# Optimization experiments

Hardware: AMD Instinct MI355X
Metric: run time of the kernel (lower is better)

The kernel has to match this reference:

```python
import jax, jax.numpy as jnp
import numpy as np

D_MODEL = 1024
N_HEADS = 16
HEAD_DIM = D_MODEL // N_HEADS


def setup_inputs() -> dict:
    key = jax.random.key(0)
    ks = jax.random.split(key, 5)
    B, S = 4, 2048
    scale = 1.0 / np.sqrt(D_MODEL)
    return {
        "x": jax.random.normal(ks[0], (B, S, D_MODEL), dtype=jnp.float32),
        "wq": jax.random.normal(ks[1], (D_MODEL, D_MODEL), dtype=jnp.float32) * scale,
        "wk": jax.random.normal(ks[2], (D_MODEL, D_MODEL), dtype=jnp.float32) * scale,
        "wv": jax.random.normal(ks[3], (D_MODEL, D_MODEL), dtype=jnp.float32) * scale,
        "wo": jax.random.normal(ks[4], (D_MODEL, D_MODEL), dtype=jnp.float32) * scale,
    }


def reference(x, wq, wk, wv, wo):
    B, S, _ = x.shape
    # projections: x @ W.T, then split heads -> [B, H, S, hd]
    def split_heads(t):
        return t.reshape(B, S, N_HEADS, HEAD_DIM).transpose(0, 2, 1, 3)

    q = split_heads(x @ wq.T)
    k = split_heads(x @ wk.T)
    v = split_heads(x @ wv.T)

    # scores [B, H, S, S], causal mask, stable softmax
    score = jnp.einsum("bhqd,bhkd->bhqk", q, k) / np.sqrt(HEAD_DIM)
    causal = jnp.tril(jnp.ones((S, S), dtype=bool))
    score = jnp.where(causal, score, -jnp.inf)
    attn = jax.nn.softmax(score, axis=-1)

    out = jnp.einsum("bhqk,bhkd->bhqd", attn, v)
    out = out.transpose(0, 2, 1, 3).reshape(B, S, D_MODEL)
    return out @ wo.T
```

## Files before the change

kernel.cpp:

```cpp
#include <hip/hip_runtime.h>
#include <type_traits>


typedef unsigned short u16;
typedef __attribute__((ext_vector_type(8))) short s8;
typedef __attribute__((ext_vector_type(4))) float f4;

__device__ __forceinline__ u16 f2bf(float f) {
    union { float f; unsigned u; } v; v.f = f;
    unsigned r = v.u + 0x7fffu + ((v.u >> 16) & 1u);
    return (u16)(r >> 16);
}

__device__ __forceinline__ unsigned pack_bf2(float a, float b) {
    return __builtin_amdgcn_perm(__float_as_uint(b), __float_as_uint(a),
                                 0x07060302u);
}

__device__ __forceinline__ void cp16(const void* g, void* l) {
    __builtin_amdgcn_global_load_lds(
        (const __attribute__((address_space(1))) unsigned int*)g,
        (__attribute__((address_space(3))) unsigned int*)l, 16, 0, 0);
}

__device__ __forceinline__ s8 load8f(const float* p) {
    const float4 lo = *(const float4*)p;
    const float4 hi = *(const float4*)(p + 4);
    s8 r;
    r[0] = (short)f2bf(lo.x); r[1] = (short)f2bf(lo.y);
    r[2] = (short)f2bf(lo.z); r[3] = (short)f2bf(lo.w);
    r[4] = (short)f2bf(hi.x); r[5] = (short)f2bf(hi.y);
    r[6] = (short)f2bf(hi.z); r[7] = (short)f2bf(hi.w);
    return r;
}

__global__ __launch_bounds__(256)
void f32_to_bf16(const float* __restrict__ in, u16* __restrict__ out, int n8)
{
    const int i = blockIdx.x * 256 + threadIdx.x;
    if (i < n8) *(s8*)(out + (size_t)i * 8) = load8f(in + (size_t)i * 8);
}

__global__ __launch_bounds__(256)
void cvt_w3(const float* __restrict__ a, const float* __restrict__ b2,
            const float* __restrict__ c3, u16* __restrict__ o, int per)
{
    const int y = blockIdx.y;
    const float* src = (y == 0) ? a : ((y == 1) ? b2 : c3);
    u16* dst = o + (size_t)y * per;
    const int i = blockIdx.x * 256 + threadIdx.x;
    *(s8*)(dst + (size_t)i * 8) = load8f(src + (size_t)i * 8);
}

template<typename TC>
__global__ __launch_bounds__(256)
void gemm_bb(const u16* __restrict__ A,
             const u16* __restrict__ W0, const u16* __restrict__ W1,
             const u16* __restrict__ W2,
             TC* __restrict__ C0, TC* __restrict__ C1,
             u16* __restrict__ VT, int K, float cscale)
{
    __shared__ u16 As[128 * 32];
    __shared__ u16 Bs[128 * 32];

    const int t  = threadIdx.x;
    const int bm = blockIdx.x;
    const int nglob = blockIdx.y * 128;

    const u16* W; int nloc, mode;
    if (nglob < 1024)      { W = W0; nloc = nglob;        mode = 0; }
    else if (nglob < 2048) { W = W1; nloc = nglob - 1024; mode = 1; }
    else                   { W = W2; nloc = nglob - 2048; mode = 2; }

    const int lane = t & 63, w = t >> 6;
    const int wm = (w >> 1) * 64, wn = (w & 1) * 64;
    const int quad = lane >> 4, l16 = lane & 15;

    const int sc = (((lane & 3) ^ ((lane >> 3) & 3))) * 8;
    const int sr = w * 32 + (lane >> 2);
    const u16* Ag0 = A + (size_t)(bm * 128 + sr) * K + sc;
    const u16* Ag1 = Ag0 + (size_t)16 * K;
    const u16* Wg0 = W + (size_t)(nloc + sr) * K + sc;
    const u16* Wg1 = Wg0 + (size_t)16 * K;
    u16* Al0 = As + (w * 32) * 32;
    u16* Al1 = As + (w * 32 + 16) * 32;
    u16* Bl0 = Bs + (w * 32) * 32;
    u16* Bl1 = Bs + (w * 32 + 16) * 32;

    const int ca = (quad ^ ((l16 >> 1) & 3)) * 8;

    f4 acc[4][4];
    for (int i = 0; i < 4; i++)
        for (int j = 0; j < 4; j++)
            acc[i][j] = (f4){0.f, 0.f, 0.f, 0.f};

    for (int k0 = 0; k0 < K; k0 += 32) {
        __syncthreads();
        cp16(Ag0 + k0, Al0);
        cp16(Ag1 + k0, Al1);
        cp16(Wg0 + k0, Bl0);
        cp16(Wg1 + k0, Bl1);
        __syncthreads();

        s8 af[4], bf[4];
        for (int i = 0; i < 4; i++)
            af[i] = *(const s8*)&As[(wm + i * 16 + l16) * 32 + ca];
        for (int j = 0; j < 4; j++)
            bf[j] = *(const s8*)&Bs[(wn + j * 16 + l16) * 32 + ca];
        for (int i = 0; i < 4; i++)
            for (int j = 0; j < 4; j++)
                acc[i][j] = __builtin_amdgcn_mfma_f32_16x16x32_bf16(
                                af[i], bf[j], acc[i][j], 0, 0, 0);
    }

    if (mode == 2) {
        for (int i = 0; i < 4; i++) {
            const int row0 = bm * 128 + wm + i * 16 + quad * 4;
            const int b = row0 >> 11, s = row0 & 2047;
            for (int j = 0; j < 4; j++) {
                const int n = nloc + wn + j * 16 + l16;
                const int h = n >> 6, d = n & 63;
                unsigned lo = ((unsigned)f2bf(acc[i][j][1]) << 16) | f2bf(acc[i][j][0]);
                unsigned hi = ((unsigned)f2bf(acc[i][j][3]) << 16) | f2bf(acc[i][j][2]);
                *(uint2*)(VT + ((size_t)((b * 16 + h) * 64 + d)) * 2048 + s) =
                    make_uint2(lo, hi);
            }
        }
    } else {
        TC* C = (mode == 0) ? C0 : C1;
        const float cs = (mode == 0) ? cscale : 1.0f;
        for (int i = 0; i < 4; i++) {
            const int row = bm * 128 + wm + i * 16 + quad * 4;
            for (int j = 0; j < 4; j++) {
                const int col = nloc + wn + j * 16 + l16;
                for (int r = 0; r < 4; r++) {
                    const float val = acc[i][j][r] * cs;
                    if constexpr (std::is_same<TC, float>::value)
                        C[(size_t)(row + r) * 1024 + col] = val;
                    else
                        C[(size_t)(row + r) * 1024 + col] = f2bf(val);
                }
            }
        }
    }
}

#define PSTR 72

__global__ __launch_bounds__(256)
void attn256(const u16* __restrict__ Q, const u16* __restrict__ K,
             const u16* __restrict__ Vt, u16* __restrict__ O)
{
    __shared__ u16 Ks[64 * 64];
    __shared__ u16 Vs[64 * 64];
    __shared__ u16 Ps[4][64 * PSTR];

    const int h  = blockIdx.x;
    const int b  = blockIdx.y;
    const int QBMAP[8] = {7, 6, 5, 4, 0, 1, 2, 3};
    const int qb = QBMAP[blockIdx.z];

    const int t = threadIdx.x, lane = t & 63, w = t >> 6;
    const int quad = lane >> 4, l16 = lane & 15;
    const int colH = h * 64;
    const size_t rowQ0 = (size_t)b * 2048 + qb * 256 + w * 64;

    s8 qf[4][2];
    for (int i = 0; i < 4; i++)
        for (int kk = 0; kk < 2; kk++)
            qf[i][kk] = *(const s8*)&Q[(rowQ0 + i * 16 + l16) * 1024 +
                                       colH + kk * 32 + quad * 8];

    s8 ones;
    for (int e = 0; e < 8; e++) ones[e] = (short)0x3F80;

    f4 o_acc[4][4];
    f4 l_acc[4];
    for (int i = 0; i < 4; i++) {
        l_acc[i] = (f4){0.f, 0.f, 0.f, 0.f};
        for (int j = 0; j < 4; j++)
            o_acc[i][j] = (f4){0.f, 0.f, 0.f, 0.f};
    }

    const int ktmax_blk = qb * 4 + 4;
    const int ktmax_w   = qb * 4 + w + 1;

    const int vrow = lane >> 3;
    const int scc  = ((lane & 7) ^ vrow) * 8;
    const int r0   = w * 16 + vrow;
    const u16* Kg0 = K  + ((size_t)b * 2048 + r0) * 1024 + colH + scc;
    const u16* Kg1 = Kg0 + (size_t)8 * 1024;
    const u16* Vg0 = Vt + ((size_t)(b * 16 + h) * 64 + r0) * 2048 + scc;
    const u16* Vg1 = Vg0 + (size_t)8 * 2048;
    const int lds_off = (lane & 7) * 8;
    u16* Kl0 = Ks + (w * 16 + vrow) * 64 + lds_off;
    u16* Kl1 = Ks + (w * 16 + 8 + vrow) * 64 + lds_off;
    u16* Vl0 = Vs + (w * 16 + vrow) * 64 + lds_off;
    u16* Vl1 = Vs + (w * 16 + 8 + vrow) * 64 + lds_off;

    s8 kr0 = *(const s8*)(Kg0);
    s8 kr1 = *(const s8*)(Kg1);
    s8 vr0 = *(const s8*)(Vg0);
    s8 vr1 = *(const s8*)(Vg1);

    for (int kt = 0; kt < ktmax_blk; ++kt) {
        __syncthreads();
        *(s8*)Kl0 = kr0;
        *(s8*)Kl1 = kr1;
        *(s8*)Vl0 = vr0;
        *(s8*)Vl1 = vr1;
        __syncthreads();

        if (kt + 1 < ktmax_blk) {
            kr0 = *(const s8*)(Kg0 + (size_t)(kt + 1) * 65536);
            kr1 = *(const s8*)(Kg1 + (size_t)(kt + 1) * 65536);
            vr0 = *(const s8*)(Vg0 + (kt + 1) * 64);
            vr1 = *(const s8*)(Vg1 + (kt + 1) * 64);
        }

        if (kt < ktmax_w) {
            f4 sa[4][4];
            for (int j = 0; j < 4; j++)
                for (int i = 0; i < 4; i++)
                    sa[j][i] = (f4){0.f, 0.f, 0.f, 0.f};
            for (int kk = 0; kk < 2; kk++) {
                s8 kf[4];
                for (int j = 0; j < 4; j++)
                    kf[j] = *(const s8*)&Ks[(j * 16 + l16) * 64 +
                                            (((kk * 4 + quad) ^ (l16 & 7)) * 8)];
                for (int j = 0; j < 4; j++)
                    for (int i = 0; i < 4; i++)
                        sa[j][i] = __builtin_amdgcn_mfma_f32_16x16x32_bf16(
                                       kf[j], qf[i][kk], sa[j][i], 0, 0, 0);
            }

            const bool diag = (kt == ktmax_w - 1);
            for (int i = 0; i < 4; i++) {
                const int q_l = i * 16 + l16;
                for (int j = 0; j < 4; j++) {
                    const int kv0 = j * 16 + quad * 4;
                    float p0 = exp2f(sa[j][i][0]);
                    float p1 = exp2f(sa[j][i][1]);
                    float p2 = exp2f(sa[j][i][2]);
                    float p3 = exp2f(sa[j][i][3]);
                    if (diag) {
                        if (kv0 + 0 > q_l) p0 = 0.f;
                        if (kv0 + 1 > q_l) p1 = 0.f;
                        if (kv0 + 2 > q_l) p2 = 0.f;
                        if (kv0 + 3 > q_l) p3 = 0.f;
                    }
                    *(uint2*)&Ps[w][q_l * PSTR + kv0] =
                        make_uint2(pack_bf2(p0, p1), pack_bf2(p2, p3));
                }
            }

            for (int kk = 0; kk < 2; kk++) {
                s8 pf[4], vf[4];
                for (int i = 0; i < 4; i++)
                    pf[i] = *(const s8*)&Ps[w][(i * 16 + l16) * PSTR +
                                               kk * 32 + quad * 8];
                for (int jd = 0; jd < 4; jd++)
                    vf[jd] = *(const s8*)&Vs[(jd * 16 + l16) * 64 +
                                             (((kk * 4 + quad) ^ (l16 & 7)) * 8)];
                for (int i = 0; i < 4; i++)
                    l_acc[i] = __builtin_amdgcn_mfma_f32_16x16x32_bf16(
                                   pf[i], ones, l_acc[i], 0, 0, 0);
                for (int i = 0; i < 4; i++)
                    for (int jd = 0; jd < 4; jd++)
                        o_acc[i][jd] = __builtin_amdgcn_mfma_f32_16x16x32_bf16(
                                           pf[i], vf[jd], o_acc[i][jd], 0, 0, 0);
            }
        }
    }

    for (int i = 0; i < 4; i++) {
        float rinv[4];
        for (int r = 0; r < 4; r++) rinv[r] = 1.0f / l_acc[i][r];
        for (int jd = 0; jd < 4; jd++)
            for (int r = 0; r < 4; r++) {
                const size_t row = rowQ0 + i * 16 + quad * 4 + r;
                O[row * 1024 + colH + jd * 16 + l16] =
                    f2bf(o_acc[i][jd][r] * rinv[r]);
            }
    }
}

extern "C" void kernel_launch(void* const* d_in, const int* in_sizes, int n_in,
                              void* d_out, int out_size, void* d_ws, size_t ws_size,
                              hipStream_t stream)
{
    const float* x  = (const float*)d_in[0];
    const float* wq = (const float*)d_in[1];
    const float* wk = (const float*)d_in[2];
    const float* wv = (const float*)d_in[3];
    const float* wo = (const float*)d_in[4];
    float* out = (float*)d_out;

    const size_t MD = (size_t)8192 * 1024;
    const size_t WD = (size_t)1024 * 1024;
    u16* Qb  = (u16*)d_ws;
    u16* Kb  = Qb + MD;
    u16* Vtb = Kb + MD;
    u16* Xb  = Vtb + MD;
    u16* Wqkv = (u16*)d_out;
    u16* Ob  = Qb;
    u16* Wob = Kb;

    f32_to_bf16<<<4096, 256, 0, stream>>>(x, Xb, (int)(MD / 8));

    cvt_w3<<<dim3(512, 3), 256, 0, stream>>>(wq, wk, wv, Wqkv, (int)WD);

    gemm_bb<u16><<<dim3(64, 24), 256, 0, stream>>>(
        Xb, Wqkv, Wqkv + WD, Wqkv + 2 * WD, Qb, Kb, Vtb, 1024, 0.18033688f);

    attn256<<<dim3(16, 4, 8), 256, 0, stream>>>(Qb, Kb, Vtb, Ob);

    f32_to_bf16<<<512, 256, 0, stream>>>(wo, Wob, (int)(WD / 8));

    gemm_bb<float><<<dim3(64, 8), 256, 0, stream>>>(
        Ob, Wob, Wob, Wob, out, out, nullptr, 1024, 1.0f);
}
```

Baseline: 296.8 us.

## Pair mirrored 32-row query strips per wave and load K/V directly into LDS

The attention kernel is restructured so each wave handles two 32-row query strips, one short causal strip and its mirror long one (63-s and s). This evens out the causal work across waves and blocks, and the grid becomes batch*heads by 8 pair groups. K/V tiles now go from global memory straight into LDS through global_load_lds, replacing the register-staged prefetch of the next tile. In exchange, the overlap of next-tile loads with compute is lost, and each wave holds half as many query rows, so every K/V tile staged in LDS feeds fewer MFMAs.

```diff
diff --git a/kernel.cpp b/kernel.cpp
--- a/kernel.cpp
+++ b/kernel.cpp
@@ -148,42 +148,28 @@
 #define PSTR 72
 
 __global__ __launch_bounds__(256)
-void attn256(const u16* __restrict__ Q, const u16* __restrict__ K,
-             const u16* __restrict__ Vt, u16* __restrict__ O)
+void attn_pair(const u16* __restrict__ Q, const u16* __restrict__ K,
+               const u16* __restrict__ Vt, u16* __restrict__ O)
 {
     __shared__ u16 Ks[64 * 64];
     __shared__ u16 Vs[64 * 64];
-    __shared__ u16 Ps[4][64 * PSTR];
-
-    const int h  = blockIdx.x;
-    const int b  = blockIdx.y;
-    const int QBMAP[8] = {7, 6, 5, 4, 0, 1, 2, 3};
-    const int qb = QBMAP[blockIdx.z];
+    __shared__ u16 Ps[4][32 * PSTR];
+
+    const int bh = blockIdx.x;
+    const int p  = blockIdx.y;
+    const int h  = bh & 15, b = bh >> 4;
 
     const int t = threadIdx.x, lane = t & 63, w = t >> 6;
     const int quad = lane >> 4, l16 = lane & 15;
     const int colH = h * 64;
-    const size_t rowQ0 = (size_t)b * 2048 + qb * 256 + w * 64;
-
-    s8 qf[4][2];
-    for (int i = 0; i < 4; i++)
-        for (int kk = 0; kk < 2; kk++)
-            qf[i][kk] = *(const s8*)&Q[(rowQ0 + i * 16 + l16) * 1024 +
-                                       colH + kk * 32 + quad * 8];
+    const int s_idx = p * 4 + w;
+
+    const int q32ph[2] = {63 - s_idx, s_idx};
+    const int kwav[2]  = {(63 - s_idx) / 2 + 1, s_idx / 2 + 1};
+    const int kblk[2]  = {(63 - 4 * p) / 2 + 1, (4 * p + 3) / 2 + 1};
 
     s8 ones;
     for (int e = 0; e < 8; e++) ones[e] = (short)0x3F80;
-
-    f4 o_acc[4][4];
-    f4 l_acc[4];
-    for (int i = 0; i < 4; i++) {
-        l_acc[i] = (f4){0.f, 0.f, 0.f, 0.f};
-        for (int j = 0; j < 4; j++)
-            o_acc[i][j] = (f4){0.f, 0.f, 0.f, 0.f};
-    }
-
-    const int ktmax_blk = qb * 4 + 4;
-    const int ktmax_w   = qb * 4 + w + 1;
 
     const int vrow = lane >> 3;
     const int scc  = ((lane & 7) ^ vrow) * 8;
@@ -192,36 +178,42 @@
     const u16* Kg1 = Kg0 + (size_t)8 * 1024;
     const u16* Vg0 = Vt + ((size_t)(b * 16 + h) * 64 + r0) * 2048 + scc;
     const u16* Vg1 = Vg0 + (size_t)8 * 2048;
-    const int lds_off = (lane & 7) * 8;
-    u16* Kl0 = Ks + (w * 16 + vrow) * 64 + lds_off;
-    u16* Kl1 = Ks + (w * 16 + 8 + vrow) * 64 + lds_off;
-    u16* Vl0 = Vs + (w * 16 + vrow) * 64 + lds_off;
-    u16* Vl1 = Vs + (w * 16 + 8 + vrow) * 64 + lds_off;
-
-    s8 kr0 = *(const s8*)(Kg0);
-    s8 kr1 = *(const s8*)(Kg1);
-    s8 vr0 = *(const s8*)(Vg0);
-    s8 vr1 = *(const s8*)(Vg1);
-
-    for (int kt = 0; kt < ktmax_blk; ++kt) {
-        __syncthreads();
-        *(s8*)Kl0 = kr0;
-        *(s8*)Kl1 = kr1;
-        *(s8*)Vl0 = vr0;
-        *(s8*)Vl1 = vr1;
-        __syncthreads();
-
-        if (kt + 1 < ktmax_blk) {
-            kr0 = *(const s8*)(Kg0 + (size_t)(kt + 1) * 65536);
-            kr1 = *(const s8*)(Kg1 + (size_t)(kt + 1) * 65536);
-            vr0 = *(const s8*)(Vg0 + (kt + 1) * 64);
-            vr1 = *(const s8*)(Vg1 + (kt + 1) * 64);
-        }
-
-        if (kt < ktmax_w) {
-            f4 sa[4][4];
+    u16* Kl0 = Ks + (w * 16) * 64;      u16* Kl1 = Ks + (w * 16 + 8) * 64;
+    u16* Vl0 = Vs + (w * 16) * 64;      u16* Vl1 = Vs + (w * 16 + 8) * 64;
+
+    for (int ph = 0; ph < 2; ++ph) {
+        const int q32 = q32ph[ph];
+        const size_t rowQ0 = (size_t)b * 2048 + q32 * 32;
+
+        s8 qf[2][2];
+        for (int i = 0; i < 2; i++)
+            for (int kk = 0; kk < 2; kk++)
+                qf[i][kk] = *(const s8*)&Q[(rowQ0 + i * 16 + l16) * 1024 +
+                                           colH + kk * 32 + quad * 8];
+
+        f4 o_acc[2][4];
+        f4 l_acc[2];
+        for (int i = 0; i < 2; i++) {
+            l_acc[i] = (f4){0.f, 0.f, 0.f, 0.f};
             for (int j = 0; j < 4; j++)
-                for (int i = 0; i < 4; i++)
+                o_acc[i][j] = (f4){0.f, 0.f, 0.f, 0.f};
+        }
+
+        const int ktw = kwav[ph];
+        const int ktb = kblk[ph];
+
+        for (int kt = 0; kt < ktb; ++kt) {
+            __syncthreads();
+            cp16(Kg0 + (size_t)kt * 65536, Kl0);
+            cp16(Kg1 + (size_t)kt * 65536, Kl1);
+            cp16(Vg0 + kt * 64, Vl0);
+            cp16(Vg1 + kt * 64, Vl1);
+            __syncthreads();
+            if (kt >= ktw) continue;
+
+            f4 sa[4][2];
+            for (int j = 0; j < 4; j++)
+                for (int i = 0; i < 2; i++)
                     sa[j][i] = (f4){0.f, 0.f, 0.f, 0.f};
             for (int kk = 0; kk < 2; kk++) {
                 s8 kf[4];
@@ -229,59 +221,60 @@
                     kf[j] = *(const s8*)&Ks[(j * 16 + l16) * 64 +
                                             (((kk * 4 + quad) ^ (l16 & 7)) * 8)];
                 for (int j = 0; j < 4; j++)
-                    for (int i = 0; i < 4; i++)
+                    for (int i = 0; i < 2; i++)
                         sa[j][i] = __builtin_amdgcn_mfma_f32_16x16x32_bf16(
                                        kf[j], qf[i][kk], sa[j][i], 0, 0, 0);
             }
 
-            const bool diag = (kt == ktmax_w - 1);
-            for (int i = 0; i < 4; i++) {
+            const bool diag = (kt == ktw - 1);
+            for (int i = 0; i < 2; i++) {
                 const int q_l = i * 16 + l16;
+                const int q_g = q32 * 32 + q_l;
                 for (int j = 0; j < 4; j++) {
-                    const int kv0 = j * 16 + quad * 4;
+                    const int kv0 = kt * 64 + j * 16 + quad * 4;
                     float p0 = exp2f(sa[j][i][0]);
                     float p1 = exp2f(sa[j][i][1]);
                     float p2 = exp2f(sa[j][i][2]);
                     float p3 = exp2f(sa[j][i][3]);
                     if (diag) {
-                        if (kv0 + 0 > q_l) p0 = 0.f;
-                        if (kv0 + 1 > q_l) p1 = 0.f;
-                        if (kv0 + 2 > q_l) p2 = 0.f;
-                        if (kv0 + 3 > q_l) p3 = 0.f;
+                        if (kv0 + 0 > q_g) p0 = 0.f;
+                        if (kv0 + 1 > q_g) p1 = 0.f;
+                        if (kv0 + 2 > q_g) p2 = 0.f;
+                        if (kv0 + 3 > q_g) p3 = 0.f;
                     }
-                    *(uint2*)&Ps[w][q_l * PSTR + kv0] =
+                    *(uint2*)&Ps[w][q_l * PSTR + j * 16 + quad * 4] =
                         make_uint2(pack_bf2(p0, p1), pack_bf2(p2, p3));
                 }
             }
 
             for (int kk = 0; kk < 2; kk++) {
-                s8 pf[4], vf[4];
-                for (int i = 0; i < 4; i++)
+                s8 pf[2], vf[4];
+                for (int i = 0; i < 2; i++)
                     pf[i] = *(const s8*)&Ps[w][(i * 16 + l16) * PSTR +
                                                kk * 32 + quad * 8];
                 for (int jd = 0; jd < 4; jd++)
                     vf[jd] = *(const s8*)&Vs[(jd * 16 + l16) * 64 +
                                              (((kk * 4 + quad) ^ (l16 & 7)) * 8)];
-                for (int i = 0; i < 4; i++)
+                for (int i = 0; i < 2; i++)
                     l_acc[i] = __builtin_amdgcn_mfma_f32_16x16x32_bf16(
                                    pf[i], ones, l_acc[i], 0, 0, 0);
-                for (int i = 0; i < 4; i++)
+                for (int i = 0; i < 2; i++)
                     for (int jd = 0; jd < 4; jd++)
                         o_acc[i][jd] = __builtin_amdgcn_mfma_f32_16x16x32_bf16(
                                            pf[i], vf[jd], o_acc[i][jd], 0, 0, 0);
             }
         }
-    }
-
-    for (int i = 0; i < 4; i++) {
-        float rinv[4];
-        for (int r = 0; r < 4; r++) rinv[r] = 1.0f / l_acc[i][r];
-        for (int jd = 0; jd < 4; jd++)
-            for (int r = 0; r < 4; r++) {
-                const size_t row = rowQ0 + i * 16 + quad * 4 + r;
-                O[row * 1024 + colH + jd * 16 + l16] =
-                    f2bf(o_acc[i][jd][r] * rinv[r]);
-            }
+
+        for (int i = 0; i < 2; i++) {
+            float rinv[4];
+            for (int r = 0; r < 4; r++) rinv[r] = 1.0f / l_acc[i][r];
+            for (int jd = 0; jd < 4; jd++)
+                for (int r = 0; r < 4; r++) {
+                    const size_t row = rowQ0 + i * 16 + quad * 4 + r;
+                    O[row * 1024 + colH + jd * 16 + l16] =
+                        f2bf(o_acc[i][jd][r] * rinv[r]);
+                }
+        }
     }
 }
 
@@ -313,7 +306,7 @@
     gemm_bb<u16><<<dim3(64, 24), 256, 0, stream>>>(
         Xb, Wqkv, Wqkv + WD, Wqkv + 2 * WD, Qb, Kb, Vtb, 1024, 0.18033688f);
 
-    attn256<<<dim3(16, 4, 8), 256, 0, stream>>>(Qb, Kb, Vtb, Ob);
+    attn_pair<<<dim3(64, 8), 256, 0, stream>>>(Qb, Kb, Vtb, Ob);
 
     f32_to_bf16<<<512, 256, 0, stream>>>(wo, Wob, (int)(WD / 8));
 
```

Result: faster. 271.3 us (-8.6%).
